# Performance work log

Measured on AMD Instinct MI355X. Metric: run time of the kernel, lower is better.

Reference implementation:

```python
import jax, jax.numpy as jnp
import numpy as np

M, K, N = 32, 8192, 8192  # tokens, in_features, out_features
PACK = 8  # int4 nibbles per int32


def setup_inputs() -> dict:
    key = jax.random.key(0)
    k1, k2, k3, k4 = jax.random.split(key, 4)
    x = (jax.random.normal(k1, (M, K), dtype=jnp.float32)).astype(jnp.float16)
    # packed int4 weights: 8 signed nibbles per int32, [N, K//8]
    b_packed = jax.random.randint(k2, (N, K // PACK), 0, 2147483647, dtype=jnp.int32)
    # rowwise fp16 scales (meta), one per output row; small positive values
    scales = (jax.random.uniform(k3, (N,), dtype=jnp.float32) * 0.01 + 1e-4).astype(jnp.float16)
    bias = (jax.random.normal(k4, (N,), dtype=jnp.float32) * 0.01).astype(jnp.float16)
    return {"x": x, "b_packed": b_packed, "scales": scales, "bias": bias}


def _unpack_int4(b_packed):
    # b_packed: [N, K//8] int32 -> signed int4 values in [-8, 7], shape [N, K]
    shifts = (jnp.arange(PACK, dtype=jnp.int32) * 4)  # [8]
    nib = (b_packed[:, :, None] >> shifts) & 0xF       # [N, K//8, 8]
    q = jnp.where(nib >= 8, nib - 16, nib)             # two's-complement nibble
    return q.reshape(b_packed.shape[0], -1)            # [N, K]


def reference(x, b_packed, scales, bias):
    # Rowwise dequant: W[n, k] = q[n, k] * scale[n]  (fp16), then y = x @ W^T + bias
    q = _unpack_int4(b_packed).astype(jnp.float16)          # [N, K]
    W = q * scales[:, None]                                  # [N, K] fp16
    y = jnp.einsum('mk,nk->mn', x, W,
                   preferred_element_type=jnp.float32).astype(jnp.float16)
    y = y + bias.astype(y.dtype)
    return y
```

## Files before the change

### kernel.cpp

```cpp
#include <hip/hip_runtime.h>
#include <cstdint>

#define M_DIM 32
#define K_DIM 8192
#define N_DIM 8192

typedef _Float16 f16x8 __attribute__((ext_vector_type(8)));
typedef _Float16 f16x2 __attribute__((ext_vector_type(2)));
typedef float    f32x4 __attribute__((ext_vector_type(4)));

__device__ __forceinline__ uint32_t u4e(uint4 v, int t) {
  return (t == 0) ? v.x : (t == 1) ? v.y : (t == 2) ? v.z : v.w;
}

__device__ __forceinline__ f16x8 dq8(uint32_t w) {
  union { uint32_t u[4]; f16x8 v; } r;
  const uint32_t MASK  = 0x000F000Fu;
  const uint32_t MAGIC = 0x64086408u;
  const f16x2 magic = __builtin_bit_cast(f16x2, MAGIC);
#pragma unroll
  for (int s = 0; s < 4; ++s) {
    uint32_t t = ((w >> (4 * s)) & MASK) ^ MAGIC;
    f16x2 h = __builtin_bit_cast(f16x2, t) - magic;
    r.u[s] = __builtin_bit_cast(uint32_t, h);
  }
  return r.v;
}

__global__ __launch_bounds__(256) void xprep_kernel(
    const float* __restrict__ x, uint4* __restrict__ xp) {
  const int T = blockIdx.x * 256 + threadIdx.x;
  const int m = T >> 10;
  const int g = T & 1023;
  const f32x4* p = (const f32x4*)(x + (size_t)m * K_DIM + (size_t)g * 8);
  f32x4 lo = p[0], hi = p[1];
  union { uint4 q; f16x8 v; } o;
#pragma unroll
  for (int s = 0; s < 4; ++s) {
    o.v[2 * s]     = (_Float16)lo[s];
    o.v[2 * s + 1] = (_Float16)hi[s];
  }
  xp[(size_t)g * 32 + m] = o.q;
}

__global__ __launch_bounds__(1024, 4) void qgemm_xp(
    const uint32_t* __restrict__ bq,
    const uint4*    __restrict__ xp,
    const float*    __restrict__ sc,
    const float*    __restrict__ bi,
    float*          __restrict__ out) {
  __shared__ float red[16][32][33];

  const int tid  = threadIdx.x;
  const int w    = tid >> 6;
  const int lane = tid & 63;
  const int l16  = lane & 15;
  const int quad = lane >> 4;
  const int n0   = blockIdx.x << 5;

  const uint4* bq4 = (const uint4*)bq;
  const uint4* bp0 = bq4 + (size_t)(n0 + l16) * 256 + (w << 4) + quad;
  const uint4* bp1 = bp0 + (size_t)16 * 256;
  const uint4* ap  = xp + (size_t)(((w << 6) + (quad << 2)) * 32 + l16);

  uint4 b0[4], b1[4];
#pragma unroll
  for (int c = 0; c < 4; ++c) { b0[c] = bp0[c * 4]; b1[c] = bp1[c * 4]; }

  f32x4 acc00 = {0.f, 0.f, 0.f, 0.f};
  f32x4 acc01 = {0.f, 0.f, 0.f, 0.f};
  f32x4 acc10 = {0.f, 0.f, 0.f, 0.f};
  f32x4 acc11 = {0.f, 0.f, 0.f, 0.f};

  uint4 a0c = ap[0], a1c = ap[16];
#pragma unroll
  for (int g = 0; g < 16; ++g) {
    const int gn  = (g + 1) & 15;
    const int off = (((gn >> 2) * 16) + (gn & 3)) * 32;
    uint4 a0n = ap[off];
    uint4 a1n = ap[off + 16];

    const int c = g >> 2, t = g & 3;
    f16x8 fb0 = dq8(u4e(b0[c], t));
    f16x8 fb1 = dq8(u4e(b1[c], t));
    f16x8 fa0 = __builtin_bit_cast(f16x8, a0c);
    f16x8 fa1 = __builtin_bit_cast(f16x8, a1c);
    acc00 = __builtin_amdgcn_mfma_f32_16x16x32_f16(fa0, fb0, acc00, 0, 0, 0);
    acc01 = __builtin_amdgcn_mfma_f32_16x16x32_f16(fa1, fb0, acc01, 0, 0, 0);
    acc10 = __builtin_amdgcn_mfma_f32_16x16x32_f16(fa0, fb1, acc10, 0, 0, 0);
    acc11 = __builtin_amdgcn_mfma_f32_16x16x32_f16(fa1, fb1, acc11, 0, 0, 0);

    a0c = a0n; a1c = a1n;
  }

#pragma unroll
  for (int r = 0; r < 4; ++r) {
    const int mr = (quad << 2) + r;
    red[w][l16][mr]           = acc00[r];
    red[w][l16][mr + 16]      = acc01[r];
    red[w][l16 + 16][mr]      = acc10[r];
    red[w][l16 + 16][mr + 16] = acc11[r];
  }

  __syncthreads();

  const int n = tid & 31;
  const int m = tid >> 5;
  float s = 0.f;
#pragma unroll
  for (int ww = 0; ww < 16; ++ww) s += red[ww][n][m];
  const int gn = n0 + n;
  out[(size_t)m * N_DIM + gn] = fmaf(s, sc[gn], bi[gn]);
}

__global__ __launch_bounds__(512) void qgemm_direct(
    const uint32_t* __restrict__ bq, const float* __restrict__ x,
    const float* __restrict__ sc, const float* __restrict__ bi,
    float* __restrict__ out) {
  __shared__ float red[8][32][40];
  const int tid  = threadIdx.x;
  const int w    = tid >> 6;
  const int lane = tid & 63;
  const int l16  = lane & 15;
  const int quad = lane >> 4;
  const int n0   = blockIdx.x << 5;

  const uint4* bq4 = (const uint4*)bq;
  const uint4* bp0 = bq4 + (size_t)(n0 + l16) * 256 + (w << 5) + quad;
  const uint4* bp1 = bp0 + (size_t)16 * 256;
  const float* ap0 = x + (size_t)l16 * K_DIM + (w << 10) + (quad << 5);
  const float* ap1 = ap0 + (size_t)16 * K_DIM;

  f32x4 acc00 = {0.f,0.f,0.f,0.f}, acc01 = {0.f,0.f,0.f,0.f};
  f32x4 acc10 = {0.f,0.f,0.f,0.f}, acc11 = {0.f,0.f,0.f,0.f};
#pragma unroll
  for (int c = 0; c < 8; ++c) {
    const uint4 wb0 = bp0[c * 4];
    const uint4 wb1 = bp1[c * 4];
#pragma unroll
    for (int t = 0; t < 4; ++t) {
      const float* a0 = ap0 + c * 128 + t * 8;
      const float* a1 = ap1 + c * 128 + t * 8;
      f32x4 l0 = *(const f32x4*)a0, h0 = *(const f32x4*)(a0 + 4);
      f32x4 l1 = *(const f32x4*)a1, h1 = *(const f32x4*)(a1 + 4);
      f16x8 fa0, fa1;
#pragma unroll
      for (int s = 0; s < 4; ++s) {
        fa0[2*s] = (_Float16)l0[s]; fa0[2*s+1] = (_Float16)h0[s];
        fa1[2*s] = (_Float16)l1[s]; fa1[2*s+1] = (_Float16)h1[s];
      }
      f16x8 fb0 = dq8(u4e(wb0, t));
      f16x8 fb1 = dq8(u4e(wb1, t));
      acc00 = __builtin_amdgcn_mfma_f32_16x16x32_f16(fa0, fb0, acc00, 0, 0, 0);
      acc01 = __builtin_amdgcn_mfma_f32_16x16x32_f16(fa1, fb0, acc01, 0, 0, 0);
      acc10 = __builtin_amdgcn_mfma_f32_16x16x32_f16(fa0, fb1, acc10, 0, 0, 0);
      acc11 = __builtin_amdgcn_mfma_f32_16x16x32_f16(fa1, fb1, acc11, 0, 0, 0);
    }
  }
#pragma unroll
  for (int r = 0; r < 4; ++r) {
    const int mr = (quad << 2) + r;
    red[w][l16][mr]           = acc00[r];
    red[w][l16][mr + 16]      = acc01[r];
    red[w][l16 + 16][mr]      = acc10[r];
    red[w][l16 + 16][mr + 16] = acc11[r];
  }
  __syncthreads();
  const int n  = tid & 31;
  const int mh = tid >> 5;
  float s0 = 0.f, s1 = 0.f;
#pragma unroll
  for (int ww = 0; ww < 8; ++ww) { s0 += red[ww][n][mh]; s1 += red[ww][n][mh+16]; }
  const int gn = n0 + n;
  out[(size_t)mh * N_DIM + gn]        = fmaf(s0, sc[gn], bi[gn]);
  out[(size_t)(mh + 16) * N_DIM + gn] = fmaf(s1, sc[gn], bi[gn]);
}

extern "C" void kernel_launch(void* const* d_in, const int* in_sizes, int n_in,
                              void* d_out, int out_size, void* d_ws, size_t ws_size,
                              hipStream_t stream) {
  const float*    x  = (const float*)d_in[0];
  const uint32_t* bq = (const uint32_t*)d_in[1];
  const float*    sc = (const float*)d_in[2];
  const float*    bi = (const float*)d_in[3];
  float*          y  = (float*)d_out;

  const size_t XP_BYTES = (size_t)M_DIM * K_DIM * 2;
  if (ws_size >= XP_BYTES) {
    uint4* xp = (uint4*)d_ws;
    xprep_kernel<<<128, 256, 0, stream>>>(x, xp);
    qgemm_xp<<<N_DIM / 32, 1024, 0, stream>>>(bq, xp, sc, bi, y);
  } else {
    qgemm_direct<<<N_DIM / 32, 512, 0, stream>>>(bq, x, sc, bi, y);
  }
}
```

Measured before the change: 87.39 us.

## Split-K GEMM with 64-row N tiles and separate reduction kernel

Replaces the 1024-thread, 32-row-tile GEMM with a 512-thread kernel that handles 64 output rows and a quarter of K per block. Partial sums are written to workspace and a new reduce kernel combines them and applies scale and bias. The wider tile lets each activation fragment be reused across four weight row groups, and A loads are prefetched three steps ahead. The cost is an extra kernel launch plus 4 MB of partial-sum traffic through global memory.

```diff
diff --git a/kernel.cpp b/kernel.cpp
--- a/kernel.cpp
+++ b/kernel.cpp
@@ -4,6 +4,7 @@
 #define M_DIM 32
 #define K_DIM 8192
 #define N_DIM 8192
+#define MN    (M_DIM * N_DIM)
 
 typedef _Float16 f16x8 __attribute__((ext_vector_type(8)));
 typedef _Float16 f16x2 __attribute__((ext_vector_type(2)));
@@ -43,74 +44,94 @@
   xp[(size_t)g * 32 + m] = o.q;
 }
 
-__global__ __launch_bounds__(1024, 4) void qgemm_xp(
+__global__ __launch_bounds__(512, 4) void qgemm2(
     const uint32_t* __restrict__ bq,
     const uint4*    __restrict__ xp,
-    const float*    __restrict__ sc,
-    const float*    __restrict__ bi,
-    float*          __restrict__ out) {
-  __shared__ float red[16][32][33];
+    float*          __restrict__ part) {
+  __shared__ float red[8][64][33];
 
   const int tid  = threadIdx.x;
   const int w    = tid >> 6;
   const int lane = tid & 63;
   const int l16  = lane & 15;
   const int quad = lane >> 4;
-  const int n0   = blockIdx.x << 5;
-
-  const uint4* bq4 = (const uint4*)bq;
-  const uint4* bp0 = bq4 + (size_t)(n0 + l16) * 256 + (w << 4) + quad;
-  const uint4* bp1 = bp0 + (size_t)16 * 256;
-  const uint4* ap  = xp + (size_t)(((w << 6) + (quad << 2)) * 32 + l16);
-
-  uint4 b0[4], b1[4];
-#pragma unroll
-  for (int c = 0; c < 4; ++c) { b0[c] = bp0[c * 4]; b1[c] = bp1[c * 4]; }
-
-  f32x4 acc00 = {0.f, 0.f, 0.f, 0.f};
-  f32x4 acc01 = {0.f, 0.f, 0.f, 0.f};
-  f32x4 acc10 = {0.f, 0.f, 0.f, 0.f};
-  f32x4 acc11 = {0.f, 0.f, 0.f, 0.f};
-
-  uint4 a0c = ap[0], a1c = ap[16];
-#pragma unroll
-  for (int g = 0; g < 16; ++g) {
-    const int gn  = (g + 1) & 15;
-    const int off = (((gn >> 2) * 16) + (gn & 3)) * 32;
-    uint4 a0n = ap[off];
-    uint4 a1n = ap[off + 16];
-
-    const int c = g >> 2, t = g & 3;
-    f16x8 fb0 = dq8(u4e(b0[c], t));
-    f16x8 fb1 = dq8(u4e(b1[c], t));
-    f16x8 fa0 = __builtin_bit_cast(f16x8, a0c);
-    f16x8 fa1 = __builtin_bit_cast(f16x8, a1c);
-    acc00 = __builtin_amdgcn_mfma_f32_16x16x32_f16(fa0, fb0, acc00, 0, 0, 0);
-    acc01 = __builtin_amdgcn_mfma_f32_16x16x32_f16(fa1, fb0, acc01, 0, 0, 0);
-    acc10 = __builtin_amdgcn_mfma_f32_16x16x32_f16(fa0, fb1, acc10, 0, 0, 0);
-    acc11 = __builtin_amdgcn_mfma_f32_16x16x32_f16(fa1, fb1, acc11, 0, 0, 0);
-
-    a0c = a0n; a1c = a1n;
-  }
-
-#pragma unroll
-  for (int r = 0; r < 4; ++r) {
-    const int mr = (quad << 2) + r;
-    red[w][l16][mr]           = acc00[r];
-    red[w][l16][mr + 16]      = acc01[r];
-    red[w][l16 + 16][mr]      = acc10[r];
-    red[w][l16 + 16][mr + 16] = acc11[r];
-  }
+  const int ntile = blockIdx.x & 127;
+  const int kq    = blockIdx.x >> 7;
+  const int n0    = ntile << 6;
+
+  const uint4* bq4  = (const uint4*)bq;
+  const int    cb   = (kq << 6) + (w << 3) + quad;
+  uint4 b[4][2];
+#pragma unroll
+  for (int r = 0; r < 4; ++r)
+#pragma unroll
+    for (int c = 0; c < 2; ++c)
+      b[r][c] = bq4[(size_t)(n0 + r * 16 + l16) * 256 + cb + c * 4];
+
+  const int dbase = (kq << 8) + (w << 5) + (quad << 2);
+  uint4 am0[8], am1[8];
+#pragma unroll
+  for (int s = 0; s < 3; ++s) {
+    const int d = dbase + ((s >> 2) << 4) + (s & 3);
+    am0[s] = xp[d * 32 + l16];
+    am1[s] = xp[d * 32 + l16 + 16];
+  }
+
+  f32x4 acc[4][2];
+#pragma unroll
+  for (int r = 0; r < 4; ++r)
+#pragma unroll
+    for (int mt = 0; mt < 2; ++mt) acc[r][mt] = (f32x4){0.f, 0.f, 0.f, 0.f};
+
+#pragma unroll
+  for (int s = 0; s < 8; ++s) {
+    if (s < 5) {
+      const int sp = s + 3;
+      const int d  = dbase + ((sp >> 2) << 4) + (sp & 3);
+      am0[sp] = xp[d * 32 + l16];
+      am1[sp] = xp[d * 32 + l16 + 16];
+    }
+    const int c = s >> 2, t = s & 3;
+    f16x8 fa0 = __builtin_bit_cast(f16x8, am0[s]);
+    f16x8 fa1 = __builtin_bit_cast(f16x8, am1[s]);
+#pragma unroll
+    for (int r = 0; r < 4; ++r) {
+      f16x8 fb = dq8(u4e(b[r][c], t));
+      acc[r][0] = __builtin_amdgcn_mfma_f32_16x16x32_f16(fa0, fb, acc[r][0], 0, 0, 0);
+      acc[r][1] = __builtin_amdgcn_mfma_f32_16x16x32_f16(fa1, fb, acc[r][1], 0, 0, 0);
+    }
+  }
+
+#pragma unroll
+  for (int r = 0; r < 4; ++r)
+#pragma unroll
+    for (int mt = 0; mt < 2; ++mt)
+#pragma unroll
+      for (int e = 0; e < 4; ++e)
+        red[w][r * 16 + l16][mt * 16 + (quad << 2) + e] = acc[r][mt][e];
 
   __syncthreads();
 
-  const int n = tid & 31;
-  const int m = tid >> 5;
-  float s = 0.f;
-#pragma unroll
-  for (int ww = 0; ww < 16; ++ww) s += red[ww][n][m];
-  const int gn = n0 + n;
-  out[(size_t)m * N_DIM + gn] = fmaf(s, sc[gn], bi[gn]);
+  const int n  = tid & 63;
+  const int mb = tid >> 6;
+  float* pp = part + (size_t)kq * MN;
+#pragma unroll
+  for (int i = 0; i < 4; ++i) {
+    const int m = mb + (i << 3);
+    float s = 0.f;
+#pragma unroll
+    for (int ww = 0; ww < 8; ++ww) s += red[ww][n][m];
+    pp[(size_t)m * N_DIM + n0 + n] = s;
+  }
+}
+
+__global__ __launch_bounds__(256) void reduce_kernel(
+    const float* __restrict__ part, const float* __restrict__ sc,
+    const float* __restrict__ bi, float* __restrict__ out) {
+  const int idx = blockIdx.x * 256 + threadIdx.x;
+  const int n = idx & (N_DIM - 1);
+  float s = part[idx] + part[idx + MN] + part[idx + 2 * MN] + part[idx + 3 * MN];
+  out[idx] = fmaf(s, sc[n], bi[n]);
 }
 
 __global__ __launch_bounds__(512) void qgemm_direct(
@@ -185,11 +206,13 @@
   const float*    bi = (const float*)d_in[3];
   float*          y  = (float*)d_out;
 
-  const size_t XP_BYTES = (size_t)M_DIM * K_DIM * 2;
-  if (ws_size >= XP_BYTES) {
-    uint4* xp = (uint4*)d_ws;
+  const size_t WS_NEED = (size_t)5 * (1 << 20) + (1 << 20);
+  if (ws_size >= WS_NEED) {
+    uint4* xp   = (uint4*)d_ws;
+    float* part = (float*)((char*)d_ws + (1 << 20));
     xprep_kernel<<<128, 256, 0, stream>>>(x, xp);
-    qgemm_xp<<<N_DIM / 32, 1024, 0, stream>>>(bq, xp, sc, bi, y);
+    qgemm2<<<512, 512, 0, stream>>>(bq, xp, part);
+    reduce_kernel<<<MN / 256, 256, 0, stream>>>(part, sc, bi, y);
   } else {
     qgemm_direct<<<N_DIM / 32, 512, 0, stream>>>(bq, x, sc, bi, y);
   }
```

After: 91.27 us. +4.4%, slower.

## Split K in two across blocks with partial buffer and separate reduce kernel

Applied to the files above, without the earlier changes.

The main GEMM kernel now splits the K dimension into two halves, launching 512 blocks instead of 256. Each block writes unscaled partial sums to a workspace buffer, and a new reduce kernel adds the two halves and applies the scale and bias. The aim is more blocks in flight to fill the CUs and hide weight-load latency. In exchange it adds a kernel launch and a write and read of partial sums, and it needs more workspace.

```diff
diff --git a/kernel.cpp b/kernel.cpp
--- a/kernel.cpp
+++ b/kernel.cpp
@@ -4,6 +4,7 @@
 #define M_DIM 32
 #define K_DIM 8192
 #define N_DIM 8192
+#define MN    (M_DIM * N_DIM)
 
 typedef _Float16 f16x8 __attribute__((ext_vector_type(8)));
 typedef _Float16 f16x2 __attribute__((ext_vector_type(2)));
@@ -43,12 +44,10 @@
   xp[(size_t)g * 32 + m] = o.q;
 }
 
-__global__ __launch_bounds__(1024, 4) void qgemm_xp(
+__global__ __launch_bounds__(1024, 8) void qgemm9(
     const uint32_t* __restrict__ bq,
     const uint4*    __restrict__ xp,
-    const float*    __restrict__ sc,
-    const float*    __restrict__ bi,
-    float*          __restrict__ out) {
+    float*          __restrict__ part) {
   __shared__ float red[16][32][33];
 
   const int tid  = threadIdx.x;
@@ -56,33 +55,38 @@
   const int lane = tid & 63;
   const int l16  = lane & 15;
   const int quad = lane >> 4;
-  const int n0   = blockIdx.x << 5;
+  const int ntile = blockIdx.x & 255;
+  const int kq    = blockIdx.x >> 8;
+  const int n0    = ntile << 5;
 
   const uint4* bq4 = (const uint4*)bq;
-  const uint4* bp0 = bq4 + (size_t)(n0 + l16) * 256 + (w << 4) + quad;
-  const uint4* bp1 = bp0 + (size_t)16 * 256;
-  const uint4* ap  = xp + (size_t)(((w << 6) + (quad << 2)) * 32 + l16);
-
-  uint4 b0[4], b1[4];
-#pragma unroll
-  for (int c = 0; c < 4; ++c) { b0[c] = bp0[c * 4]; b1[c] = bp1[c * 4]; }
+  const int    cb  = (kq << 7) + (w << 3) + quad;
+  uint4 b[2][2];
+#pragma unroll
+  for (int r = 0; r < 2; ++r)
+#pragma unroll
+    for (int c = 0; c < 2; ++c)
+      b[r][c] = bq4[(size_t)(n0 + r * 16 + l16) * 256 + cb + c * 4];
+
+  const int dbase = (kq << 9) + (w << 5) + (quad << 2);
+  const uint4* ap = xp + (size_t)dbase * 32;
 
   f32x4 acc00 = {0.f, 0.f, 0.f, 0.f};
   f32x4 acc01 = {0.f, 0.f, 0.f, 0.f};
   f32x4 acc10 = {0.f, 0.f, 0.f, 0.f};
   f32x4 acc11 = {0.f, 0.f, 0.f, 0.f};
 
-  uint4 a0c = ap[0], a1c = ap[16];
-#pragma unroll
-  for (int g = 0; g < 16; ++g) {
-    const int gn  = (g + 1) & 15;
-    const int off = (((gn >> 2) * 16) + (gn & 3)) * 32;
-    uint4 a0n = ap[off];
-    uint4 a1n = ap[off + 16];
-
-    const int c = g >> 2, t = g & 3;
-    f16x8 fb0 = dq8(u4e(b0[c], t));
-    f16x8 fb1 = dq8(u4e(b1[c], t));
+  uint4 a0c = ap[l16], a1c = ap[l16 + 16];
+#pragma unroll
+  for (int s = 0; s < 8; ++s) {
+    const int sn  = (s + 1) & 7;
+    const int off = (((sn >> 2) << 4) + (sn & 3)) * 32;
+    uint4 a0n = ap[off + l16];
+    uint4 a1n = ap[off + l16 + 16];
+
+    const int c = s >> 2, t = s & 3;
+    f16x8 fb0 = dq8(u4e(b[0][c], t));
+    f16x8 fb1 = dq8(u4e(b[1][c], t));
     f16x8 fa0 = __builtin_bit_cast(f16x8, a0c);
     f16x8 fa1 = __builtin_bit_cast(f16x8, a1c);
     acc00 = __builtin_amdgcn_mfma_f32_16x16x32_f16(fa0, fb0, acc00, 0, 0, 0);
@@ -94,12 +98,12 @@
   }
 
 #pragma unroll
-  for (int r = 0; r < 4; ++r) {
-    const int mr = (quad << 2) + r;
-    red[w][l16][mr]           = acc00[r];
-    red[w][l16][mr + 16]      = acc01[r];
-    red[w][l16 + 16][mr]      = acc10[r];
-    red[w][l16 + 16][mr + 16] = acc11[r];
+  for (int e = 0; e < 4; ++e) {
+    const int mr = (quad << 2) + e;
+    red[w][l16][mr]           = acc00[e];
+    red[w][l16][mr + 16]      = acc01[e];
+    red[w][l16 + 16][mr]      = acc10[e];
+    red[w][l16 + 16][mr + 16] = acc11[e];
   }
 
   __syncthreads();
@@ -109,8 +113,16 @@
   float s = 0.f;
 #pragma unroll
   for (int ww = 0; ww < 16; ++ww) s += red[ww][n][m];
-  const int gn = n0 + n;
-  out[(size_t)m * N_DIM + gn] = fmaf(s, sc[gn], bi[gn]);
+  part[(size_t)kq * MN + (size_t)m * N_DIM + n0 + n] = s;
+}
+
+__global__ __launch_bounds__(256) void reduce_kernel(
+    const float* __restrict__ part, const float* __restrict__ sc,
+    const float* __restrict__ bi, float* __restrict__ out) {
+  const int idx = blockIdx.x * 256 + threadIdx.x;
+  const int n = idx & (N_DIM - 1);
+  float s = part[idx] + part[idx + MN];
+  out[idx] = fmaf(s, sc[n], bi[n]);
 }
 
 __global__ __launch_bounds__(512) void qgemm_direct(
@@ -185,11 +197,13 @@
   const float*    bi = (const float*)d_in[3];
   float*          y  = (float*)d_out;
 
-  const size_t XP_BYTES = (size_t)M_DIM * K_DIM * 2;
-  if (ws_size >= XP_BYTES) {
-    uint4* xp = (uint4*)d_ws;
+  const size_t WS_NEED = (size_t)3 * (1 << 20);
+  if (ws_size >= WS_NEED) {
+    uint4* xp   = (uint4*)d_ws;
+    float* part = (float*)((char*)d_ws + (1 << 20));
     xprep_kernel<<<128, 256, 0, stream>>>(x, xp);
-    qgemm_xp<<<N_DIM / 32, 1024, 0, stream>>>(bq, xp, sc, bi, y);
+    qgemm9<<<512, 1024, 0, stream>>>(bq, xp, part);
+    reduce_kernel<<<MN / 256, 256, 0, stream>>>(part, sc, bi, y);
   } else {
     qgemm_direct<<<N_DIM / 32, 512, 0, stream>>>(bq, x, sc, bi, y);
   }
```

Measured after the change: 90.82 us. 3.9% more time.

## Stage packed int4 weights into LDS via global_load_lds before MFMA loop

Applied to the files above, without the earlier changes.

The weight tile for each 32-row block is now fetched with direct global-to-LDS DMA loads, using fully coalesced contiguous 16-byte accesses, into a padded shared buffer. Each wave then reads its slices from LDS instead of issuing strided per-lane global loads into registers. The shared buffer is reused for the cross-wave reduction after an extra barrier. The aim is better coalescing and fewer register-held loads, at the cost of about 133KB of LDS per block and additional synchronisation.

```diff
diff --git a/kernel.cpp b/kernel.cpp
--- a/kernel.cpp
+++ b/kernel.cpp
@@ -8,6 +8,13 @@
 typedef _Float16 f16x8 __attribute__((ext_vector_type(8)));
 typedef _Float16 f16x2 __attribute__((ext_vector_type(2)));
 typedef float    f32x4 __attribute__((ext_vector_type(4)));
+
+#define QSTRIDE 260
+#define QBLOCK  (32 * QSTRIDE)
+#define SMEM_DW (4 * QBLOCK)
+
+#define GPTR(p) ((const __attribute__((address_space(1))) uint4*)(p))
+#define LPTR(p) ((__attribute__((address_space(3))) uint4*)(p))
 
 __device__ __forceinline__ uint32_t u4e(uint4 v, int t) {
   return (t == 0) ? v.x : (t == 1) ? v.y : (t == 2) ? v.z : v.w;
@@ -43,13 +50,13 @@
   xp[(size_t)g * 32 + m] = o.q;
 }
 
-__global__ __launch_bounds__(1024, 4) void qgemm_xp(
+__global__ __launch_bounds__(1024, 4) void qgemm_dma(
     const uint32_t* __restrict__ bq,
     const uint4*    __restrict__ xp,
     const float*    __restrict__ sc,
     const float*    __restrict__ bi,
     float*          __restrict__ out) {
-  __shared__ float red[16][32][33];
+  __shared__ uint32_t smem[SMEM_DW];
 
   const int tid  = threadIdx.x;
   const int w    = tid >> 6;
@@ -58,48 +65,67 @@
   const int quad = lane >> 4;
   const int n0   = blockIdx.x << 5;
 
-  const uint4* bq4 = (const uint4*)bq;
-  const uint4* bp0 = bq4 + (size_t)(n0 + l16) * 256 + (w << 4) + quad;
-  const uint4* bp1 = bp0 + (size_t)16 * 256;
-  const uint4* ap  = xp + (size_t)(((w << 6) + (quad << 2)) * 32 + l16);
-
-  uint4 b0[4], b1[4];
-#pragma unroll
-  for (int c = 0; c < 4; ++c) { b0[c] = bp0[c * 4]; b1[c] = bp1[c * 4]; }
+  const uint4* bsrc = (const uint4*)bq + (size_t)n0 * 256;
+  const int qrt = w & 3;
+  const int rw  = w >> 2;
+#pragma unroll
+  for (int i = 0; i < 8; ++i) {
+    const int row = i * 4 + rw;
+    __builtin_amdgcn_global_load_lds(
+        GPTR(bsrc + i * 1024 + tid),
+        LPTR(&smem[qrt * QBLOCK + row * QSTRIDE]),
+        16, 0, 0);
+  }
+
+  const uint4* ap = xp + (size_t)(((w << 6) + (quad << 2)) * 32 + l16);
+  uint4 a0c = ap[0];
+  uint4 a1c = ap[16];
+
+  __syncthreads();
 
   f32x4 acc00 = {0.f, 0.f, 0.f, 0.f};
   f32x4 acc01 = {0.f, 0.f, 0.f, 0.f};
   f32x4 acc10 = {0.f, 0.f, 0.f, 0.f};
   f32x4 acc11 = {0.f, 0.f, 0.f, 0.f};
 
-  uint4 a0c = ap[0], a1c = ap[16];
-#pragma unroll
-  for (int g = 0; g < 16; ++g) {
-    const int gn  = (g + 1) & 15;
-    const int off = (((gn >> 2) * 16) + (gn & 3)) * 32;
-    uint4 a0n = ap[off];
-    uint4 a1n = ap[off + 16];
-
-    const int c = g >> 2, t = g & 3;
-    f16x8 fb0 = dq8(u4e(b0[c], t));
-    f16x8 fb1 = dq8(u4e(b1[c], t));
-    f16x8 fa0 = __builtin_bit_cast(f16x8, a0c);
-    f16x8 fa1 = __builtin_bit_cast(f16x8, a1c);
-    acc00 = __builtin_amdgcn_mfma_f32_16x16x32_f16(fa0, fb0, acc00, 0, 0, 0);
-    acc01 = __builtin_amdgcn_mfma_f32_16x16x32_f16(fa1, fb0, acc01, 0, 0, 0);
-    acc10 = __builtin_amdgcn_mfma_f32_16x16x32_f16(fa0, fb1, acc10, 0, 0, 0);
-    acc11 = __builtin_amdgcn_mfma_f32_16x16x32_f16(fa1, fb1, acc11, 0, 0, 0);
-
-    a0c = a0n; a1c = a1n;
-  }
-
-#pragma unroll
-  for (int r = 0; r < 4; ++r) {
-    const int mr = (quad << 2) + r;
-    red[w][l16][mr]           = acc00[r];
-    red[w][l16][mr + 16]      = acc01[r];
-    red[w][l16 + 16][mr]      = acc10[r];
-    red[w][l16 + 16][mr + 16] = acc11[r];
+  const int bbase = (w >> 2) * QBLOCK + ((w & 3) * 16 + quad) * 4;
+
+#pragma unroll
+  for (int c = 0; c < 4; ++c) {
+    const int bidx = bbase + c * 16;
+    const uint4 bb0 = *(const uint4*)&smem[bidx + l16 * QSTRIDE];
+    const uint4 bb1 = *(const uint4*)&smem[bidx + (l16 + 16) * QSTRIDE];
+#pragma unroll
+    for (int t = 0; t < 4; ++t) {
+      const int g   = c * 4 + t;
+      const int gn2 = (g + 1) & 15;
+      const int off = (((gn2 >> 2) << 4) + (gn2 & 3)) << 5;
+      uint4 a0n = ap[off];
+      uint4 a1n = ap[off + 16];
+
+      f16x8 fb0 = dq8(u4e(bb0, t));
+      f16x8 fb1 = dq8(u4e(bb1, t));
+      f16x8 fa0 = __builtin_bit_cast(f16x8, a0c);
+      f16x8 fa1 = __builtin_bit_cast(f16x8, a1c);
+      acc00 = __builtin_amdgcn_mfma_f32_16x16x32_f16(fa0, fb0, acc00, 0, 0, 0);
+      acc01 = __builtin_amdgcn_mfma_f32_16x16x32_f16(fa1, fb0, acc01, 0, 0, 0);
+      acc10 = __builtin_amdgcn_mfma_f32_16x16x32_f16(fa0, fb1, acc10, 0, 0, 0);
+      acc11 = __builtin_amdgcn_mfma_f32_16x16x32_f16(fa1, fb1, acc11, 0, 0, 0);
+
+      a0c = a0n; a1c = a1n;
+    }
+  }
+
+  __syncthreads();
+
+  float* red = (float*)smem;
+#pragma unroll
+  for (int e = 0; e < 4; ++e) {
+    const int mr = (quad << 2) + e;
+    red[(w * 32 + l16) * 33 + mr]           = acc00[e];
+    red[(w * 32 + l16) * 33 + mr + 16]      = acc01[e];
+    red[(w * 32 + l16 + 16) * 33 + mr]      = acc10[e];
+    red[(w * 32 + l16 + 16) * 33 + mr + 16] = acc11[e];
   }
 
   __syncthreads();
@@ -108,7 +134,7 @@
   const int m = tid >> 5;
   float s = 0.f;
 #pragma unroll
-  for (int ww = 0; ww < 16; ++ww) s += red[ww][n][m];
+  for (int ww = 0; ww < 16; ++ww) s += red[(ww * 32 + n) * 33 + m];
   const int gn = n0 + n;
   out[(size_t)m * N_DIM + gn] = fmaf(s, sc[gn], bi[gn]);
 }
@@ -189,7 +215,7 @@
   if (ws_size >= XP_BYTES) {
     uint4* xp = (uint4*)d_ws;
     xprep_kernel<<<128, 256, 0, stream>>>(x, xp);
-    qgemm_xp<<<N_DIM / 32, 1024, 0, stream>>>(bq, xp, sc, bi, y);
+    qgemm_dma<<<N_DIM / 32, 1024, 0, stream>>>(bq, xp, sc, bi, y);
   } else {
     qgemm_direct<<<N_DIM / 32, 512, 0, stream>>>(bq, x, sc, bi, y);
   }
```

After: 88.84 us. About the same (+1.7%).
